# Kernel tuning notes

Hardware: AMD Instinct MI355X
Metric: run time of the kernel (lower is better)

Reference implementation:

```python
import jax, jax.numpy as jnp
import numpy as np

B, S, D = 8, 1024, 1024
H = 16
DH = D // H
DFF = 4096
L = 2
EPS = 1e-6


def setup_inputs() -> dict:
    key = jax.random.key(0)
    ks = jax.random.split(key, 12)
    sc = 0.02
    x = jax.random.normal(ks[0], (B, S, D), dtype=jnp.float32)
    # causal mask: 1 where position j > i (masked), broadcast over batch/head
    mask = jnp.triu(jnp.ones((S, S), dtype=jnp.float32), k=1)[None, None]
    Wq = jax.random.normal(ks[1], (L, D, D), dtype=jnp.float32) * sc
    Wk = jax.random.normal(ks[2], (L, D, D), dtype=jnp.float32) * sc
    Wv = jax.random.normal(ks[3], (L, D, D), dtype=jnp.float32) * sc
    Wo = jax.random.normal(ks[4], (L, D, D), dtype=jnp.float32) * sc
    bq = jnp.zeros((L, D), jnp.float32)
    bk = jnp.zeros((L, D), jnp.float32)
    bv = jnp.zeros((L, D), jnp.float32)
    bo = jnp.zeros((L, D), jnp.float32)
    W1 = jax.random.normal(ks[5], (L, D, DFF), dtype=jnp.float32) * sc
    b1 = jnp.zeros((L, DFF), jnp.float32)
    W2 = jax.random.normal(ks[6], (L, DFF, D), dtype=jnp.float32) * sc
    b2 = jnp.zeros((L, D), jnp.float32)
    ln1_g = jnp.ones((L, D), jnp.float32)
    ln1_b = jnp.zeros((L, D), jnp.float32)
    ln2_g = jnp.ones((L, D), jnp.float32)
    ln2_b = jnp.zeros((L, D), jnp.float32)
    return dict(x=x, mask=mask, Wq=Wq, bq=bq, Wk=Wk, bk=bk, Wv=Wv, bv=bv,
                Wo=Wo, bo=bo, W1=W1, b1=b1, W2=W2, b2=b2,
                ln1_g=ln1_g, ln1_b=ln1_b, ln2_g=ln2_g, ln2_b=ln2_b)


def layer_norm(x, g, b):
    mu = jnp.mean(x, axis=-1, keepdims=True)
    var = jnp.mean(jnp.square(x - mu), axis=-1, keepdims=True)
    return (x - mu) * jax.lax.rsqrt(var + EPS) * g + b


def reference(x, mask, Wq, bq, Wk, bk, Wv, bv, Wo, bo, W1, b1, W2, b2,
              ln1_g, ln1_b, ln2_g, ln2_b):
    scale = 1.0 / jnp.sqrt(jnp.float32(DH))
    for l in range(L):
        # --- multi-head attention (inference mode: no dropout) ---
        q = (x @ Wq[l] + bq[l]).reshape(B, S, H, DH).transpose(0, 2, 1, 3)
        k = (x @ Wk[l] + bk[l]).reshape(B, S, H, DH).transpose(0, 2, 1, 3)
        v = (x @ Wv[l] + bv[l]).reshape(B, S, H, DH).transpose(0, 2, 1, 3)
        sim = jnp.einsum('bhqd,bhkd->bhqk', q, k) * scale + mask * (-1e9)
        attn = jax.nn.softmax(sim, axis=-1)
        o = jnp.einsum('bhqk,bhkd->bhqd', attn, v)
        o = o.transpose(0, 2, 1, 3).reshape(B, S, D)
        o = o @ Wo[l] + bo[l]
        x = layer_norm(o + x, ln1_g[l], ln1_b[l])
        # --- feed-forward network ---
        h = jax.nn.relu(x @ W1[l] + b1[l])
        f = h @ W2[l] + b2[l]
        x = layer_norm(x + f, ln2_g[l], ln2_b[l])
    return x
```

## Files before the change

kernel.cpp:

```cpp
#include <hip/hip_runtime.h>

typedef __attribute__((ext_vector_type(8))) short bf16x8;
typedef __attribute__((ext_vector_type(4))) float f32x4;
typedef unsigned short ushort_t;
typedef unsigned int uint32;

#define DEV __device__ __forceinline__

DEV ushort_t f2bf(float f) {
    uint32 u = __float_as_uint(f);
    uint32 r = (u + 0x7FFFu + ((u >> 16) & 1u)) >> 16;
    return (ushort_t)r;
}
DEV float bf2f(ushort_t h) { return __uint_as_float(((uint32)h) << 16); }

#define MFMA16(a, b, c) __builtin_amdgcn_mfma_f32_16x16x32_bf16((a), (b), (c), 0, 0, 0)

DEV void gload_lds16(const void* g, void* l) {
    __builtin_amdgcn_global_load_lds((const __attribute__((address_space(1))) void*)g,
                                     (__attribute__((address_space(3))) void*)l,
                                     16, 0, 0);
}

__global__ __launch_bounds__(256) void init_x(const float* __restrict__ xin,
                                              float* __restrict__ x,
                                              ushort_t* __restrict__ xb, int n4) {
    int i = blockIdx.x * 256 + threadIdx.x;
    if (i >= n4) return;
    float4 v = ((const float4*)xin)[i];
    ((float4*)x)[i] = v;
    ushort4 h;
    h.x = f2bf(v.x); h.y = f2bf(v.y); h.z = f2bf(v.z); h.w = f2bf(v.w);
    ((ushort4*)xb)[i] = h;
}

__global__ __launch_bounds__(256) void transpose_all(const float* __restrict__ Wq,
                                                     const float* __restrict__ Wk,
                                                     const float* __restrict__ Wv,
                                                     const float* __restrict__ Wo,
                                                     const float* __restrict__ W1,
                                                     const float* __restrict__ W2,
                                                     ushort_t* __restrict__ wqkvT,
                                                     ushort_t* __restrict__ woT,
                                                     ushort_t* __restrict__ w1T,
                                                     ushort_t* __restrict__ w2T) {
    const int l = blockIdx.y;
    const int t = blockIdx.x;
    const float* src;
    ushort_t* dst;
    int K, N, ktile, ntile;
    if (t < 4096) {
        const int which = t >> 10, tile = t & 1023;
        K = 1024; N = 1024; ktile = tile >> 5; ntile = tile & 31;
        const size_t o1 = (size_t)l * 1048576;
        if (which == 0)      { src = Wq + o1; dst = wqkvT + (size_t)l * 3145728; }
        else if (which == 1) { src = Wk + o1; dst = wqkvT + (size_t)l * 3145728 + 1048576; }
        else if (which == 2) { src = Wv + o1; dst = wqkvT + (size_t)l * 3145728 + 2097152; }
        else                 { src = Wo + o1; dst = woT + o1; }
    } else if (t < 8192) {
        const int tile = t - 4096;
        K = 1024; N = 4096; ktile = tile >> 7; ntile = tile & 127;
        src = W1 + (size_t)l * 4194304; dst = w1T + (size_t)l * 4194304;
    } else {
        const int tile = t - 8192;
        K = 4096; N = 1024; ktile = tile >> 5; ntile = tile & 31;
        src = W2 + (size_t)l * 4194304; dst = w2T + (size_t)l * 4194304;
    }
    __shared__ float tilebuf[32][33];
    const int tx = threadIdx.x, ty = threadIdx.y;
    const int nt = ntile * 32, kt = ktile * 32;
#pragma unroll
    for (int j = 0; j < 4; ++j)
        tilebuf[ty + j * 8][tx] = src[(size_t)(kt + ty + j * 8) * N + nt + tx];
    __syncthreads();
#pragma unroll
    for (int j = 0; j < 4; ++j)
        dst[(size_t)(nt + ty + j * 8) * K + kt + tx] = f2bf(tilebuf[tx][ty + j * 8]);
}

template <int BM, int MODE, int RELU>
__global__ __launch_bounds__(512, 2) void gemm8p(const ushort_t* __restrict__ A,
                                                 const ushort_t* __restrict__ BT,
                                                 const float* __restrict__ bias,
                                                 void* __restrict__ Cout,
                                                 int M, int N, int K, int gx,
                                                 ushort_t* __restrict__ qout,
                                                 ushort_t* __restrict__ kout,
                                                 ushort_t* __restrict__ vtout,
                                                 const float* __restrict__ bq,
                                                 const float* __restrict__ bk,
                                                 const float* __restrict__ bv) {
    constexpr int AH = BM / 128;
    constexpr int MREP = BM / 32;
    constexpr int MPP = MREP / 4;
    __shared__ ushort_t lds[2][(BM + 256) * 64];

    const int nwg = gridDim.x;
    const int q8 = nwg >> 3, r8 = nwg & 7;
    const int xcd = blockIdx.x & 7, idx = blockIdx.x >> 3;
    const int swz = (xcd < r8 ? xcd * (q8 + 1) : r8 * (q8 + 1) + (xcd - r8) * q8) + idx;
    const int bxi = swz % gx, byi = swz / gx;

    const int tid = threadIdx.x;
    const int w = tid >> 6, lane = tid & 63;
    const int wr = w >> 2, wc = w & 3;
    const int lr = lane & 15, lh = lane >> 4;
    const int row0 = byi * BM, col0 = bxi * 256;

    f32x4 acc[MREP][4] = {};

    const ushort_t* __restrict__ Ab = A + (size_t)row0 * K;
    const ushort_t* __restrict__ Bb = BT + (size_t)col0 * K;
    const int nt = K >> 6;

    const int r8l = lane >> 3;
    const int cu = (lane & 7) ^ r8l;

    auto stage_half = [&](const ushort_t* src, ushort_t* lbase) {
#pragma unroll
        for (int i = 0; i < 2; ++i) {
            const int rowi = (w * 2 + i) * 8 + r8l;
            gload_lds16(src + (size_t)rowi * K + cu * 8, lbase + (w * 2 + i) * 512 + lane * 8);
        }
    };
    auto Ahalf = [&](int buf, int h) -> ushort_t* { return &lds[buf][h * 8192]; };
    auto Bhalf = [&](int buf, int h) -> ushort_t* { return &lds[buf][BM * 64 + h * 8192]; };
    auto stA = [&](int kt, int h, int buf) {
        stage_half(Ab + (size_t)h * 128 * K + (size_t)kt * 64, Ahalf(buf, h));
    };
    auto stB = [&](int kt, int h, int buf) {
        stage_half(Bb + (size_t)h * 128 * K + (size_t)kt * 64, Bhalf(buf, h));
    };

    stB(0, 0, 0); stB(0, 1, 0);
    stA(0, 0, 0); if (AH == 2) stA(0, 1, 0);
    stB(1, 0, 1); stB(1, 1, 1);
    asm volatile("s_waitcnt vmcnt(4)" ::: "memory");
    __builtin_amdgcn_sched_barrier(0);
    __builtin_amdgcn_s_barrier();

    for (int t = 0; t < nt; ++t) {
        const int cb = t & 1, nb = cb ^ 1;
        bf16x8 bfrag[4][2];
#pragma unroll
        for (int p = 0; p < 4; ++p) {
            if (p == 0) {
#pragma unroll
                for (int ni = 0; ni < 4; ++ni) {
                    const int br = wc * 64 + ni * 16 + lr;
                    const ushort_t* bh = Bhalf(cb, br >> 7);
                    const int rr = br & 127;
#pragma unroll
                    for (int ks = 0; ks < 2; ++ks)
                        bfrag[ni][ks] = *(const bf16x8*)&bh[rr * 64 + (((ks * 4 + lh) ^ (rr & 7)) * 8)];
                }
            }
            bf16x8 af[MPP][2];
#pragma unroll
            for (int mm = 0; mm < MPP; ++mm) {
                const int fr = wr * (BM / 2) + (p * MPP + mm) * 16 + lr;
                const ushort_t* ah = Ahalf(cb, fr >> 7);
                const int rr = fr & 127;
#pragma unroll
                for (int ks = 0; ks < 2; ++ks)
                    af[mm][ks] = *(const bf16x8*)&ah[rr * 64 + (((ks * 4 + lh) ^ (rr & 7)) * 8)];
            }
            if (p == 0) { if (t + 1 < nt) stA(t + 1, 0, nb); }
            else if (p == 1) { if (AH == 2 && t + 1 < nt) stA(t + 1, 1, nb); }
            else if (p == 2) { if (t + 2 < nt) stB(t + 2, 0, cb); }
            else {
                if (t + 2 < nt) {
                    stB(t + 2, 1, cb);
                    asm volatile("s_waitcnt vmcnt(4)" ::: "memory");
                } else if (t + 1 < nt) {
                    asm volatile("s_waitcnt vmcnt(0)" ::: "memory");
                }
            }
            __builtin_amdgcn_sched_barrier(0);
            __builtin_amdgcn_s_barrier();
            asm volatile("s_waitcnt lgkmcnt(0)" ::: "memory");
            __builtin_amdgcn_sched_barrier(0);
            __builtin_amdgcn_s_setprio(1);
#pragma unroll
            for (int mm = 0; mm < MPP; ++mm)
#pragma unroll
                for (int ni = 0; ni < 4; ++ni)
#pragma unroll
                    for (int ks = 0; ks < 2; ++ks)
                        acc[p * MPP + mm][ni] = MFMA16(af[mm][ks], bfrag[ni][ks], acc[p * MPP + mm][ni]);
            __builtin_amdgcn_s_setprio(0);
            __builtin_amdgcn_sched_barrier(0);
            __builtin_amdgcn_s_barrier();
        }
    }
    (void)M;

#pragma unroll
    for (int mi = 0; mi < MREP; ++mi) {
#pragma unroll
        for (int ni = 0; ni < 4; ++ni) {
            const int col = col0 + wc * 64 + ni * 16 + lr;
            const int rowb = row0 + wr * (BM / 2) + mi * 16 + lh * 4;
            if (MODE == 2) {
                if (col < 1024) {
                    const float bvv = bq[col];
#pragma unroll
                    for (int r = 0; r < 4; ++r)
                        qout[(size_t)(rowb + r) * 1024 + col] = f2bf((acc[mi][ni][r] + bvv) * 0.125f);
                } else if (col < 2048) {
                    const int c = col - 1024;
                    const float bvv = bk[c];
#pragma unroll
                    for (int r = 0; r < 4; ++r)
                        kout[(size_t)(rowb + r) * 1024 + c] = f2bf(acc[mi][ni][r] + bvv);
                } else {
                    const int d = col - 2048;
                    const int h = d >> 6, dd = d & 63;
                    const int b = rowb >> 10, s = rowb & 1023;
                    const float bvv = bv[d];
                    ushort4 h4;
                    h4.x = f2bf(acc[mi][ni][0] + bvv);
                    h4.y = f2bf(acc[mi][ni][1] + bvv);
                    h4.z = f2bf(acc[mi][ni][2] + bvv);
                    h4.w = f2bf(acc[mi][ni][3] + bvv);
                    *(ushort4*)&vtout[(((size_t)(b * 16 + h) * 64 + dd) << 10) + s] = h4;
                }
            } else {
                const float bvv = bias[col];
#pragma unroll
                for (int r = 0; r < 4; ++r) {
                    float val = acc[mi][ni][r] + bvv;
                    if (RELU) val = fmaxf(val, 0.f);
                    ((ushort_t*)Cout)[(size_t)(rowb + r) * N + col] = f2bf(val);
                }
            }
        }
    }
}

__global__ __launch_bounds__(256) void attn_kernel(const ushort_t* __restrict__ q,
                                                   const ushort_t* __restrict__ k,
                                                   const ushort_t* __restrict__ vt,
                                                   ushort_t* __restrict__ o) {
    __shared__ ushort_t ktile[64 * 64];
    __shared__ ushort_t vtile[64 * 64];
    __shared__ ushort_t p_lds[4][16 * 64];

    const int bh = blockIdx.x;
    const int b = bh >> 4, h = bh & 15;
    const int qt = blockIdx.y;
    const int tid = threadIdx.x, w = tid >> 6, lane = tid & 63;
    const int lr = lane & 15, lh = lane >> 4;
    const int qbase = qt * 64 + w * 16;
    const size_t headoff = (size_t)b * 1024 * 1024 + h * 64;
    const size_t vhead = (size_t)(b * 16 + h) << 16;

    bf16x8 qf[2];
#pragma unroll
    for (int ks = 0; ks < 2; ++ks)
        qf[ks] = *(const bf16x8*)&q[headoff + (size_t)(qbase + lr) * 1024 + ks * 32 + lh * 8];

    f32x4 oacc[4] = {};
    float m[4] = {-INFINITY, -INFINITY, -INFINITY, -INFINITY};
    float ls[4] = {0.f, 0.f, 0.f, 0.f};

    const int srow = tid >> 3;
    const int scolb = (tid & 7) * 16;
    const int swz0 = ((srow & 7) << 4);
    char* const kbase = (char*)ktile;
    char* const vbase = (char*)vtile;
    char* const kw0 = kbase + srow * 128 + (scolb ^ swz0);
    char* const kw1 = kbase + (srow + 32) * 128 + (scolb ^ swz0);
    char* const vw0 = vbase + srow * 128 + (scolb ^ swz0);
    char* const vw1 = vbase + (srow + 32) * 128 + (scolb ^ swz0);
    const ushort_t* kg = k + headoff + (size_t)srow * 1024 + (tid & 7) * 8;
    const ushort_t* vg = vt + vhead + (size_t)srow * 1024 + (tid & 7) * 8;

    const int jmaxw = qbase + 15;
    const int jend = qt * 64 + 63;

    bf16x8 sk0 = *(const bf16x8*)&kg[0];
    bf16x8 sk1 = *(const bf16x8*)&kg[32 * 1024];
    bf16x8 sv0 = *(const bf16x8*)&vg[0];
    bf16x8 sv1 = *(const bf16x8*)&vg[32 * 1024];

    for (int j0 = 0; j0 <= jend; j0 += 64) {
        __syncthreads();
        *(bf16x8*)kw0 = sk0;
        *(bf16x8*)kw1 = sk1;
        *(bf16x8*)vw0 = sv0;
        *(bf16x8*)vw1 = sv1;
        __syncthreads();
        if (j0 + 64 <= jend) {
            sk0 = *(const bf16x8*)&kg[(size_t)(j0 + 64) * 1024];
            sk1 = *(const bf16x8*)&kg[(size_t)(j0 + 64) * 1024 + 32 * 1024];
            sv0 = *(const bf16x8*)&vg[j0 + 64];
            sv1 = *(const bf16x8*)&vg[32 * 1024 + j0 + 64];
        }

        if (j0 <= jmaxw) {
            f32x4 s[4] = {{0,0,0,0},{0,0,0,0},{0,0,0,0},{0,0,0,0}};
#pragma unroll
            for (int kt = 0; kt < 4; ++kt) {
                const int row = kt * 16 + lr;
                const int rswz = ((row & 7) << 4);
#pragma unroll
                for (int ks = 0; ks < 2; ++ks) {
                    bf16x8 kf = *(const bf16x8*)(kbase + row * 128 + ((ks * 64 + lh * 16) ^ rswz));
                    s[kt] = MFMA16(qf[ks], kf, s[kt]);
                }
            }
            if (j0 + 63 > qbase) {
#pragma unroll
                for (int kt = 0; kt < 4; ++kt)
#pragma unroll
                    for (int r = 0; r < 4; ++r)
                        s[kt][r] = ((j0 + kt * 16 + lr) <= (qbase + lh * 4 + r)) ? s[kt][r] : -1e9f;
            }
#pragma unroll
            for (int r = 0; r < 4; ++r) {
                float pm = fmaxf(fmaxf(s[0][r], s[1][r]), fmaxf(s[2][r], s[3][r]));
                pm = fmaxf(pm, __shfl_xor(pm, 1, 16));
                pm = fmaxf(pm, __shfl_xor(pm, 2, 16));
                pm = fmaxf(pm, __shfl_xor(pm, 4, 16));
                pm = fmaxf(pm, __shfl_xor(pm, 8, 16));
                const float mn = fmaxf(m[r], pm);
                const float corr = __expf(m[r] - mn);
                m[r] = mn;
                float p0 = __expf(s[0][r] - mn);
                float p1 = __expf(s[1][r] - mn);
                float p2 = __expf(s[2][r] - mn);
                float p3 = __expf(s[3][r] - mn);
                s[0][r] = p0; s[1][r] = p1; s[2][r] = p2; s[3][r] = p3;
                float ps = (p0 + p1) + (p2 + p3);
                ps += __shfl_xor(ps, 1, 16);
                ps += __shfl_xor(ps, 2, 16);
                ps += __shfl_xor(ps, 4, 16);
                ps += __shfl_xor(ps, 8, 16);
                ls[r] = ls[r] * corr + ps;
                oacc[0][r] *= corr; oacc[1][r] *= corr;
                oacc[2][r] *= corr; oacc[3][r] *= corr;
            }
            char* const pb = (char*)p_lds[w];
#pragma unroll
            for (int r = 0; r < 4; ++r) {
                const int qrow = lh * 4 + r;
                const int qswz = ((qrow & 7) << 4);
#pragma unroll
                for (int kt = 0; kt < 4; ++kt)
                    *(ushort_t*)(pb + qrow * 128 + ((kt * 32 + lr * 2) ^ qswz)) = f2bf(s[kt][r]);
            }
            const int pswz = ((lr & 7) << 4);
            bf16x8 pa0 = *(const bf16x8*)(pb + lr * 128 + ((lh * 16) ^ pswz));
            bf16x8 pa1 = *(const bf16x8*)(pb + lr * 128 + ((64 + lh * 16) ^ pswz));
#pragma unroll
            for (int dt = 0; dt < 4; ++dt) {
                const int vrow = dt * 16 + lr;
                const int vswz = ((vrow & 7) << 4);
                bf16x8 vf0 = *(const bf16x8*)(vbase + vrow * 128 + ((lh * 16) ^ vswz));
                oacc[dt] = MFMA16(pa0, vf0, oacc[dt]);
                bf16x8 vf1 = *(const bf16x8*)(vbase + vrow * 128 + ((64 + lh * 16) ^ vswz));
                oacc[dt] = MFMA16(pa1, vf1, oacc[dt]);
            }
        }
    }

    float inv[4];
#pragma unroll
    for (int r = 0; r < 4; ++r) inv[r] = 1.f / ls[r];
#pragma unroll
    for (int dt = 0; dt < 4; ++dt)
#pragma unroll
        for (int r = 0; r < 4; ++r) {
            const int row = qbase + lh * 4 + r;
            o[headoff + (size_t)row * 1024 + dt * 16 + lr] = f2bf(oacc[dt][r] * inv[r]);
        }
}

__global__ __launch_bounds__(256) void add_ln(const ushort_t* __restrict__ t,
                                              float* __restrict__ x,
                                              const float* __restrict__ g,
                                              const float* __restrict__ bb,
                                              ushort_t* __restrict__ xb) {
    const int row = blockIdx.x, tid = threadIdx.x;
    const int lane = tid & 63, w = tid >> 6;
    const size_t base = (size_t)row * 1024;
    ushort4 tv = ((const ushort4*)(t + base))[tid];
    float4 xv = ((const float4*)(x + base))[tid];
    float v0 = bf2f(tv.x) + xv.x, v1 = bf2f(tv.y) + xv.y;
    float v2 = bf2f(tv.z) + xv.z, v3 = bf2f(tv.w) + xv.w;
    float s = v0 + v1 + v2 + v3;
    float sq = v0 * v0 + v1 * v1 + v2 * v2 + v3 * v3;
#pragma unroll
    for (int off = 32; off >= 1; off >>= 1) {
        s += __shfl_xor(s, off);
        sq += __shfl_xor(sq, off);
    }
    __shared__ float red[8];
    if (lane == 0) { red[w] = s; red[4 + w] = sq; }
    __syncthreads();
    s = red[0] + red[1] + red[2] + red[3];
    sq = red[4] + red[5] + red[6] + red[7];
    const float mu = s * (1.f / 1024.f);
    const float var = sq * (1.f / 1024.f) - mu * mu;
    const float rs = rsqrtf(var + 1e-6f);
    float4 gv = ((const float4*)g)[tid];
    float4 bv = ((const float4*)bb)[tid];
    float y0 = (v0 - mu) * rs * gv.x + bv.x;
    float y1 = (v1 - mu) * rs * gv.y + bv.y;
    float y2 = (v2 - mu) * rs * gv.z + bv.z;
    float y3 = (v3 - mu) * rs * gv.w + bv.w;
    float4 yo; yo.x = y0; yo.y = y1; yo.z = y2; yo.w = y3;
    ((float4*)(x + base))[tid] = yo;
    ushort4 hh;
    hh.x = f2bf(y0); hh.y = f2bf(y1); hh.z = f2bf(y2); hh.w = f2bf(y3);
    ((ushort4*)(xb + base))[tid] = hh;
}

extern "C" void kernel_launch(void* const* d_in, const int* in_sizes, int n_in,
                              void* d_out, int out_size, void* d_ws, size_t ws_size,
                              hipStream_t stream) {
    (void)in_sizes; (void)n_in; (void)out_size; (void)ws_size;
    const int B = 8, S = 1024, D = 1024, DFF = 4096, L = 2;
    const int M = B * S;

    const float* x_in = (const float*)d_in[0];
    const float* Wq = (const float*)d_in[2];
    const float* bq = (const float*)d_in[3];
    const float* Wk = (const float*)d_in[4];
    const float* bk = (const float*)d_in[5];
    const float* Wv = (const float*)d_in[6];
    const float* bv = (const float*)d_in[7];
    const float* Wo = (const float*)d_in[8];
    const float* bo = (const float*)d_in[9];
    const float* W1 = (const float*)d_in[10];
    const float* b1 = (const float*)d_in[11];
    const float* W2 = (const float*)d_in[12];
    const float* b2 = (const float*)d_in[13];
    const float* ln1g = (const float*)d_in[14];
    const float* ln1b = (const float*)d_in[15];
    const float* ln2g = (const float*)d_in[16];
    const float* ln2b = (const float*)d_in[17];

    float* x = (float*)d_out;
    char* ws = (char*)d_ws;
    const size_t MB = 1024 * 1024;
    ushort_t* wqkvT = (ushort_t*)(ws + 0 * MB);
    ushort_t* woT = (ushort_t*)(ws + 12 * MB);
    ushort_t* w1T = (ushort_t*)(ws + 16 * MB);
    ushort_t* w2T = (ushort_t*)(ws + 32 * MB);
    ushort_t* xb  = (ushort_t*)(ws + 48 * MB);
    ushort_t* qb  = (ushort_t*)(ws + 64 * MB);
    ushort_t* kb  = (ushort_t*)(ws + 80 * MB);
    ushort_t* vtb = (ushort_t*)(ws + 96 * MB);
    ushort_t* ob  = (ushort_t*)(ws + 112 * MB);
    ushort_t* hb  = (ushort_t*)(ws + 64 * MB);
    ushort_t* tb  = (ushort_t*)(ws + 128 * MB);

    init_x<<<M * D / 4 / 256, 256, 0, stream>>>(x_in, x, xb, M * D / 4);
    transpose_all<<<dim3(12288, L), dim3(32, 8), 0, stream>>>(
        Wq, Wk, Wv, Wo, W1, W2, wqkvT, woT, w1T, w2T);

    for (int l = 0; l < L; ++l) {
        const size_t wOff = (size_t)l * D * D;
        const size_t bOff = (size_t)l * D;
        gemm8p<128, 2, 0><<<dim3(768), 512, 0, stream>>>(
            xb, wqkvT + (size_t)l * 3 * D * D, nullptr, nullptr, M, 3 * D, D, 12,
            qb, kb, vtb, bq + bOff, bk + bOff, bv + bOff);
        attn_kernel<<<dim3(B * 16, S / 64), 256, 0, stream>>>(qb, kb, vtb, ob);
        gemm8p<128, 1, 0><<<dim3(256), 512, 0, stream>>>(
            ob, woT + wOff, bo + bOff, tb, M, D, D, 4,
            nullptr, nullptr, nullptr, nullptr, nullptr, nullptr);
        add_ln<<<M, 256, 0, stream>>>(tb, x, ln1g + bOff, ln1b + bOff, xb);
        gemm8p<256, 1, 1><<<dim3(512), 512, 0, stream>>>(
            xb, w1T + (size_t)l * D * DFF, b1 + (size_t)l * DFF, hb, M, DFF, D, 16,
            nullptr, nullptr, nullptr, nullptr, nullptr, nullptr);
        gemm8p<128, 1, 0><<<dim3(256), 512, 0, stream>>>(
            hb, w2T + (size_t)l * DFF * D, b2 + bOff, tb, M, D, DFF, 4,
            nullptr, nullptr, nullptr, nullptr, nullptr, nullptr);
        add_ln<<<M, 256, 0, stream>>>(tb, x, ln2g + bOff, ln2b + bOff, xb);
    }
}
```

Baseline: 735.3 us.

## Keep residual stream in bf16 and stage V-transpose stores through LDS

```diff
diff --git a/kernel.cpp b/kernel.cpp
--- a/kernel.cpp
+++ b/kernel.cpp
@@ -23,15 +23,13 @@
 }
 
 __global__ __launch_bounds__(256) void init_x(const float* __restrict__ xin,
-                                              float* __restrict__ x,
-                                              ushort_t* __restrict__ xb, int n4) {
+                                              ushort_t* __restrict__ xr, int n4) {
     int i = blockIdx.x * 256 + threadIdx.x;
     if (i >= n4) return;
     float4 v = ((const float4*)xin)[i];
-    ((float4*)x)[i] = v;
     ushort4 h;
     h.x = f2bf(v.x); h.y = f2bf(v.y); h.z = f2bf(v.z); h.w = f2bf(v.w);
-    ((ushort4*)xb)[i] = h;
+    ((ushort4*)xr)[i] = h;
 }
 
 __global__ __launch_bounds__(256) void transpose_all(const float* __restrict__ Wq,
@@ -195,43 +193,61 @@
     }
     (void)M;
 
-#pragma unroll
-    for (int mi = 0; mi < MREP; ++mi) {
-#pragma unroll
-        for (int ni = 0; ni < 4; ++ni) {
-            const int col = col0 + wc * 64 + ni * 16 + lr;
-            const int rowb = row0 + wr * (BM / 2) + mi * 16 + lh * 4;
-            if (MODE == 2) {
-                if (col < 1024) {
-                    const float bvv = bq[col];
-#pragma unroll
-                    for (int r = 0; r < 4; ++r)
-                        qout[(size_t)(rowb + r) * 1024 + col] = f2bf((acc[mi][ni][r] + bvv) * 0.125f);
-                } else if (col < 2048) {
-                    const int c = col - 1024;
-                    const float bvv = bk[c];
-#pragma unroll
-                    for (int r = 0; r < 4; ++r)
-                        kout[(size_t)(rowb + r) * 1024 + c] = f2bf(acc[mi][ni][r] + bvv);
+    if (MODE == 2 && col0 >= 2048) {
+        ushort_t* vb = &lds[0][0] + w * 4096;
+        const int hglob = (col0 - 2048 + wc * 64) >> 6;
+        const int bidx = row0 >> 10;
+        const int srow0 = (row0 & 1023) + wr * 64;
+#pragma unroll
+        for (int mi = 0; mi < MREP; ++mi) {
+#pragma unroll
+            for (int ni = 0; ni < 4; ++ni) {
+                const int dd = ni * 16 + lr;
+                const float bvv = bv[(hglob << 6) + dd];
+                ushort4 h4;
+                h4.x = f2bf(acc[mi][ni][0] + bvv);
+                h4.y = f2bf(acc[mi][ni][1] + bvv);
+                h4.z = f2bf(acc[mi][ni][2] + bvv);
+                h4.w = f2bf(acc[mi][ni][3] + bvv);
+                const int sb = mi * 32 + lh * 8;
+                *(ushort4*)((char*)vb + dd * 128 + (sb ^ ((dd & 3) << 4))) = h4;
+            }
+        }
+        const int ddl = lane >> 3, s8 = lane & 7;
+#pragma unroll
+        for (int j = 0; j < 8; ++j) {
+            const int dd = j * 8 + ddl;
+            bf16x8 rowv = *(const bf16x8*)((char*)vb + dd * 128 + ((s8 * 16) ^ ((dd & 3) << 4)));
+            *(bf16x8*)&vtout[(((size_t)(bidx * 16 + hglob) * 64 + dd) << 10) + srow0 + s8 * 8] = rowv;
+        }
+    } else {
+#pragma unroll
+        for (int mi = 0; mi < MREP; ++mi) {
+#pragma unroll
+            for (int ni = 0; ni < 4; ++ni) {
+                const int col = col0 + wc * 64 + ni * 16 + lr;
+                const int rowb = row0 + wr * (BM / 2) + mi * 16 + lh * 4;
+                if (MODE == 2) {
+                    if (col < 1024) {
+                        const float bvv = bq[col];
+#pragma unroll
+                        for (int r = 0; r < 4; ++r)
+                            qout[(size_t)(rowb + r) * 1024 + col] = f2bf((acc[mi][ni][r] + bvv) * 0.125f);
+                    } else {
+                        const int c = col - 1024;
+                        const float bvv = bk[c];
+#pragma unroll
+                        for (int r = 0; r < 4; ++r)
+                            kout[(size_t)(rowb + r) * 1024 + c] = f2bf(acc[mi][ni][r] + bvv);
+                    }
                 } else {
-                    const int d = col - 2048;
-                    const int h = d >> 6, dd = d & 63;
-                    const int b = rowb >> 10, s = rowb & 1023;
-                    const float bvv = bv[d];
-                    ushort4 h4;
-                    h4.x = f2bf(acc[mi][ni][0] + bvv);
-                    h4.y = f2bf(acc[mi][ni][1] + bvv);
-                    h4.z = f2bf(acc[mi][ni][2] + bvv);
-                    h4.w = f2bf(acc[mi][ni][3] + bvv);
-                    *(ushort4*)&vtout[(((size_t)(b * 16 + h) * 64 + dd) << 10) + s] = h4;
-                }
-            } else {
-                const float bvv = bias[col];
-#pragma unroll
-                for (int r = 0; r < 4; ++r) {
-                    float val = acc[mi][ni][r] + bvv;
-                    if (RELU) val = fmaxf(val, 0.f);
-                    ((ushort_t*)Cout)[(size_t)(rowb + r) * N + col] = f2bf(val);
+                    const float bvv = bias[col];
+#pragma unroll
+                    for (int r = 0; r < 4; ++r) {
+                        float val = acc[mi][ni][r] + bvv;
+                        if (RELU) val = fmaxf(val, 0.f);
+                        ((ushort_t*)Cout)[(size_t)(rowb + r) * N + col] = f2bf(val);
+                    }
                 }
             }
         }
@@ -377,18 +393,19 @@
         }
 }
 
+template <int LAST>
 __global__ __launch_bounds__(256) void add_ln(const ushort_t* __restrict__ t,
-                                              float* __restrict__ x,
+                                              ushort_t* __restrict__ xr,
                                               const float* __restrict__ g,
                                               const float* __restrict__ bb,
-                                              ushort_t* __restrict__ xb) {
+                                              float* __restrict__ out) {
     const int row = blockIdx.x, tid = threadIdx.x;
     const int lane = tid & 63, w = tid >> 6;
     const size_t base = (size_t)row * 1024;
     ushort4 tv = ((const ushort4*)(t + base))[tid];
-    float4 xv = ((const float4*)(x + base))[tid];
-    float v0 = bf2f(tv.x) + xv.x, v1 = bf2f(tv.y) + xv.y;
-    float v2 = bf2f(tv.z) + xv.z, v3 = bf2f(tv.w) + xv.w;
+    ushort4 xv = ((const ushort4*)(xr + base))[tid];
+    float v0 = bf2f(tv.x) + bf2f(xv.x), v1 = bf2f(tv.y) + bf2f(xv.y);
+    float v2 = bf2f(tv.z) + bf2f(xv.z), v3 = bf2f(tv.w) + bf2f(xv.w);
     float s = v0 + v1 + v2 + v3;
     float sq = v0 * v0 + v1 * v1 + v2 * v2 + v3 * v3;
 #pragma unroll
@@ -410,11 +427,14 @@
     float y1 = (v1 - mu) * rs * gv.y + bv.y;
     float y2 = (v2 - mu) * rs * gv.z + bv.z;
     float y3 = (v3 - mu) * rs * gv.w + bv.w;
-    float4 yo; yo.x = y0; yo.y = y1; yo.z = y2; yo.w = y3;
-    ((float4*)(x + base))[tid] = yo;
-    ushort4 hh;
-    hh.x = f2bf(y0); hh.y = f2bf(y1); hh.z = f2bf(y2); hh.w = f2bf(y3);
-    ((ushort4*)(xb + base))[tid] = hh;
+    if (LAST) {
+        float4 yo; yo.x = y0; yo.y = y1; yo.z = y2; yo.w = y3;
+        ((float4*)(out + base))[tid] = yo;
+    } else {
+        ushort4 hh;
+        hh.x = f2bf(y0); hh.y = f2bf(y1); hh.z = f2bf(y2); hh.w = f2bf(y3);
+        ((ushort4*)(xr + base))[tid] = hh;
+    }
 }
 
 extern "C" void kernel_launch(void* const* d_in, const int* in_sizes, int n_in,
@@ -442,14 +462,14 @@
     const float* ln2g = (const float*)d_in[16];
     const float* ln2b = (const float*)d_in[17];
 
-    float* x = (float*)d_out;
+    float* out = (float*)d_out;
     char* ws = (char*)d_ws;
     const size_t MB = 1024 * 1024;
     ushort_t* wqkvT = (ushort_t*)(ws + 0 * MB);
     ushort_t* woT = (ushort_t*)(ws + 12 * MB);
     ushort_t* w1T = (ushort_t*)(ws + 16 * MB);
     ushort_t* w2T = (ushort_t*)(ws + 32 * MB);
-    ushort_t* xb  = (ushort_t*)(ws + 48 * MB);
+    ushort_t* xr  = (ushort_t*)(ws + 48 * MB);
     ushort_t* qb  = (ushort_t*)(ws + 64 * MB);
     ushort_t* kb  = (ushort_t*)(ws + 80 * MB);
     ushort_t* vtb = (ushort_t*)(ws + 96 * MB);
@@ -457,7 +477,7 @@
     ushort_t* hb  = (ushort_t*)(ws + 64 * MB);
     ushort_t* tb  = (ushort_t*)(ws + 128 * MB);
 
-    init_x<<<M * D / 4 / 256, 256, 0, stream>>>(x_in, x, xb, M * D / 4);
+    init_x<<<M * D / 4 / 256, 256, 0, stream>>>(x_in, xr, M * D / 4);
     transpose_all<<<dim3(12288, L), dim3(32, 8), 0, stream>>>(
         Wq, Wk, Wv, Wo, W1, W2, wqkvT, woT, w1T, w2T);
 
@@ -465,19 +485,22 @@
         const size_t wOff = (size_t)l * D * D;
         const size_t bOff = (size_t)l * D;
         gemm8p<128, 2, 0><<<dim3(768), 512, 0, stream>>>(
-            xb, wqkvT + (size_t)l * 3 * D * D, nullptr, nullptr, M, 3 * D, D, 12,
+            xr, wqkvT + (size_t)l * 3 * D * D, nullptr, nullptr, M, 3 * D, D, 12,
             qb, kb, vtb, bq + bOff, bk + bOff, bv + bOff);
         attn_kernel<<<dim3(B * 16, S / 64), 256, 0, stream>>>(qb, kb, vtb, ob);
         gemm8p<128, 1, 0><<<dim3(256), 512, 0, stream>>>(
             ob, woT + wOff, bo + bOff, tb, M, D, D, 4,
             nullptr, nullptr, nullptr, nullptr, nullptr, nullptr);
-        add_ln<<<M, 256, 0, stream>>>(tb, x, ln1g + bOff, ln1b + bOff, xb);
+        add_ln<0><<<M, 256, 0, stream>>>(tb, xr, ln1g + bOff, ln1b + bOff, nullptr);
         gemm8p<256, 1, 1><<<dim3(512), 512, 0, stream>>>(
-            xb, w1T + (size_t)l * D * DFF, b1 + (size_t)l * DFF, hb, M, DFF, D, 16,
+            xr, w1T + (size_t)l * D * DFF, b1 + (size_t)l * DFF, hb, M, DFF, D, 16,
             nullptr, nullptr, nullptr, nullptr, nullptr, nullptr);
         gemm8p<128, 1, 0><<<dim3(256), 512, 0, stream>>>(
             hb, w2T + (size_t)l * DFF * D, b2 + bOff, tb, M, D, DFF, 4,
             nullptr, nullptr, nullptr, nullptr, nullptr, nullptr);
-        add_ln<<<M, 256, 0, stream>>>(tb, x, ln2g + bOff, ln2b + bOff, xb);
-    }
-}
+        if (l == L - 1)
+            add_ln<1><<<M, 256, 0, stream>>>(tb, xr, ln2g + bOff, ln2b + bOff, out);
+        else
+            add_ln<0><<<M, 256, 0, stream>>>(tb, xr, ln2g + bOff, ln2b + bOff, nullptr);
+    }
+}
```

Result: faster. 699.8 us (-4.8%).
